# Kernel tuning notes

Hardware: AMD Instinct MI355X
Metric: run time of the kernel (lower is better)

## Reference

```python
import jax, jax.numpy as jnp
import numpy as np

H = 12          # num heads
D = 768         # embed dim
HD = D // H     # head dim
SCALE = HD ** -0.5
NEG = -(3.0 ** 39)  # matches torch's triu(1) * -3.0**39 mask value


def setup_inputs() -> dict:
    key = jax.random.key(0)
    ks = jax.random.split(key, 9)
    B, S = 4, 1024
    lim = 1.0 / np.sqrt(D)
    def lin(k):
        kw, kb = jax.random.split(k)
        W = jax.random.uniform(kw, (D, D), jnp.float32, -lim, lim)  # [out,in]
        b = jax.random.uniform(kb, (D,), jnp.float32, -lim, lim)
        return W, b
    Wq, bq = lin(ks[0]); Wk, bk = lin(ks[1]); Wv, bv = lin(ks[2]); Wo, bo = lin(ks[3])
    hidden_states = jax.random.normal(ks[4], (B, S, D), jnp.float32)
    return {"hidden_states": hidden_states,
            "Wq": Wq, "bq": bq, "Wk": Wk, "bk": bk,
            "Wv": Wv, "bv": bv, "Wo": Wo, "bo": bo}


def reference(hidden_states, Wq, bq, Wk, bk, Wv, bv, Wo, bo):
    B, S, _ = hidden_states.shape
    split = lambda x: x.reshape(B, S, H, HD).transpose(0, 2, 1, 3)  # [B,H,S,HD]
    q = split(hidden_states @ Wq.T + bq) * SCALE
    k = split(hidden_states @ Wk.T + bk)
    v = split(hidden_states @ Wv.T + bv)
    scores = jnp.einsum('bhqd,bhkd->bhqk', q, k)
    causal_mask = jnp.triu(jnp.full((S, S), NEG, hidden_states.dtype), k=1)
    scores = scores + causal_mask  # broadcast over [B,H]
    probs = jax.nn.softmax(scores, axis=-1)
    out = jnp.einsum('bhqk,bhkd->bhqd', probs, v)
    out = out.transpose(0, 2, 1, 3).reshape(B, S, H * HD)
    return out @ Wo.T + bo
```

## Files before the change

kernel.cpp:

```cpp
#include <hip/hip_runtime.h>

#define NH 12
#define DM 768
#define HD 64
#define BB 4
#define SS 1024
#define MTOT (BB*SS)
#define ATT_SCALE 0.125f
#define NEGMASK (-4.0525551530189755e18f)

typedef __attribute__((ext_vector_type(8))) short short8;
typedef __attribute__((ext_vector_type(4))) float floatx4;
typedef __attribute__((ext_vector_type(4))) unsigned short ushort4v;

__device__ __forceinline__ float bf2f(unsigned short u){
    union { unsigned int i; float f; } x; x.i = ((unsigned int)u) << 16; return x.f;
}
__device__ __forceinline__ unsigned short f2bf(float f){
    union { float f; unsigned int i; } x; x.f = f;
    unsigned int i = x.i;
    return (unsigned short)((i + 0x7FFFu + ((i >> 16) & 1u)) >> 16);
}

#define XQ4 (MTOT*DM/4)
#define WQ4 (DM*DM/4)

__global__ __launch_bounds__(256) void convert_bf16(
    const float* __restrict__ X,
    const float* __restrict__ Wq, const float* __restrict__ Wk,
    const float* __restrict__ Wv, const float* __restrict__ Wo,
    unsigned short* __restrict__ Xb,
    unsigned short* __restrict__ Wqb, unsigned short* __restrict__ Wkb,
    unsigned short* __restrict__ Wvb, unsigned short* __restrict__ Wob)
{
    const int idx = blockIdx.x * 256 + threadIdx.x;
    const float* s; unsigned short* d; int off;
    if (idx < XQ4) { s = X; d = Xb; off = idx; }
    else {
        const int r = idx - XQ4;
        const int wsel = r / WQ4;
        off = r - wsel * WQ4;
        s = (wsel==0)?Wq:(wsel==1)?Wk:(wsel==2)?Wv:Wo;
        d = (wsel==0)?Wqb:(wsel==1)?Wkb:(wsel==2)?Wvb:Wob;
    }
    const float4 v = ((const float4*)s)[off];
    ushort4v o;
    o[0] = f2bf(v.x); o[1] = f2bf(v.y); o[2] = f2bf(v.z); o[3] = f2bf(v.w);
    ((ushort4v*)d)[off] = o;
}

__global__ __launch_bounds__(256) void qkv_mfma(
    const unsigned short* __restrict__ Xb,
    const unsigned short* __restrict__ Wqb,
    const unsigned short* __restrict__ Wkb,
    const unsigned short* __restrict__ Wvb,
    const float* __restrict__ bq, const float* __restrict__ bk,
    const float* __restrict__ bv,
    unsigned short* __restrict__ qout,
    unsigned short* __restrict__ kout,
    unsigned short* __restrict__ vout)
{
    const int which = blockIdx.z;
    const int n0 = blockIdx.x * 64;
    const int m0 = blockIdx.y * 128;
    const unsigned short* W = (which==0) ? Wqb : (which==1) ? Wkb : Wvb;
    const float* bias = (which==0) ? bq : (which==1) ? bk : bv;
    const float scl = (which==0) ? ATT_SCALE : 1.0f;

    __shared__ unsigned short As[128*32];
    __shared__ unsigned short Bs[64*32];

    const int t = threadIdx.x;
    const int w = t >> 6, lane = t & 63;
    const int c = lane & 15, g = lane >> 4;
    const int wr = w >> 1, wc = w & 1;

    floatx4 acc[4][2] = {};

    const int srow = lane >> 2;
    const int ske  = (lane & 3) * 8;

    for (int k0 = 0; k0 < DM; k0 += 32) {
        __syncthreads();
        #pragma unroll
        for (int j = 0; j < 2; ++j) {
            const int row = w*32 + j*16 + srow;
            __builtin_amdgcn_global_load_lds(
                (const __attribute__((address_space(1))) unsigned int*)
                    (Xb + (size_t)(m0 + row) * DM + k0 + ske),
                (__attribute__((address_space(3))) unsigned int*)
                    (As + (w*32 + j*16) * 32),
                16, 0, 0);
        }
        {
            const int row = w*16 + srow;
            __builtin_amdgcn_global_load_lds(
                (const __attribute__((address_space(1))) unsigned int*)
                    (W + (size_t)(n0 + row) * DM + k0 + ske),
                (__attribute__((address_space(3))) unsigned int*)
                    (Bs + (w*16) * 32),
                16, 0, 0);
        }
        __syncthreads();

        short8 af[4], bfr[2];
        #pragma unroll
        for (int mi = 0; mi < 4; ++mi)
            af[mi] = *(const short8*)(As + (wr*64 + mi*16 + c)*32 + g*8);
        #pragma unroll
        for (int ni = 0; ni < 2; ++ni)
            bfr[ni] = *(const short8*)(Bs + (wc*32 + ni*16 + c)*32 + g*8);
        #pragma unroll
        for (int mi = 0; mi < 4; ++mi)
            #pragma unroll
            for (int ni = 0; ni < 2; ++ni)
                acc[mi][ni] = __builtin_amdgcn_mfma_f32_16x16x32_bf16(
                    af[mi], bfr[ni], acc[mi][ni], 0, 0, 0);
    }

    #pragma unroll
    for (int mi = 0; mi < 4; ++mi) {
        #pragma unroll
        for (int r = 0; r < 4; ++r) {
            const int m = m0 + wr*64 + mi*16 + g*4 + r;
            const int b = m >> 10, s = m & 1023;
            #pragma unroll
            for (int ni = 0; ni < 2; ++ni) {
                const int n = n0 + wc*32 + ni*16 + c;
                const int h = n >> 6, hd = n & 63;
                const float val = (acc[mi][ni][r] + bias[n]) * scl;
                if (which == 2)
                    vout[(((size_t)(b*NH + h))*HD + hd)*SS + s] = f2bf(val);
                else if (which == 1)
                    kout[(((size_t)(b*NH + h))*SS + s)*HD + hd] = f2bf(val);
                else
                    qout[(((size_t)(b*NH + h))*SS + s)*HD + hd] = f2bf(val);
            }
        }
    }
}

__global__ __launch_bounds__(64) void attn_mfma(
    const unsigned short* __restrict__ Q,
    const unsigned short* __restrict__ K,
    const unsigned short* __restrict__ VT,
    unsigned short* __restrict__ O)
{
    const int idx = blockIdx.x;
    const int bh  = idx % 48;
    const int z   = 63 - (idx / 48);
    const int q0  = z * 16;

    const unsigned short* Qp  = Q  + (size_t)bh * SS * HD;
    const unsigned short* Kp  = K  + (size_t)bh * SS * HD;
    const unsigned short* VTp = VT + (size_t)bh * HD * SS;

    __shared__ unsigned short Pl[16 * 72];

    const int lane = threadIdx.x;
    const int c    = lane & 15;
    const int g    = lane >> 4;

    short8 qf[2];
    #pragma unroll
    for (int st = 0; st < 2; ++st)
        qf[st] = *(const short8*)(Qp + (size_t)(q0 + c) * HD + g*8 + 32*st);

    floatx4 Oacc[4] = {};
    float m_r[4], l_r[4];
    #pragma unroll
    for (int r = 0; r < 4; ++r) { m_r[r] = -INFINITY; l_r[r] = 0.0f; }

    const int ntile = z/4 + 1;
    for (int kt = 0; kt < ntile; ++kt) {
        const int k0 = kt * 64;

        short8 kf[4][2], vf[2][4];
        #pragma unroll
        for (int nf = 0; nf < 4; ++nf)
            #pragma unroll
            for (int st = 0; st < 2; ++st)
                kf[nf][st] = *(const short8*)(Kp + (size_t)(k0 + nf*16 + c) * HD + g*8 + 32*st);
        #pragma unroll
        for (int st = 0; st < 2; ++st)
            #pragma unroll
            for (int nf = 0; nf < 4; ++nf)
                vf[st][nf] = *(const short8*)(VTp + (size_t)(nf*16 + c) * SS + k0 + g*8 + 32*st);

        floatx4 Sacc[4] = {};
        #pragma unroll
        for (int nf = 0; nf < 4; ++nf)
            #pragma unroll
            for (int st = 0; st < 2; ++st)
                Sacc[nf] = __builtin_amdgcn_mfma_f32_16x16x32_bf16(qf[st], kf[nf][st], Sacc[nf], 0, 0, 0);

        if (kt == ntile - 1) {
            #pragma unroll
            for (int nf = 0; nf < 4; ++nf) {
                const int col = k0 + nf*16 + c;
                #pragma unroll
                for (int r = 0; r < 4; ++r) {
                    const int row = q0 + g*4 + r;
                    if (col > row) Sacc[nf][r] += NEGMASK;
                }
            }
        }

        #pragma unroll
        for (int r = 0; r < 4; ++r) {
            float mx = fmaxf(fmaxf(Sacc[0][r], Sacc[1][r]),
                             fmaxf(Sacc[2][r], Sacc[3][r]));
            #pragma unroll
            for (int msk = 1; msk < 16; msk <<= 1)
                mx = fmaxf(mx, __shfl_xor(mx, msk, 64));
            const float mnew = fmaxf(m_r[r], mx);
            const float alpha = __expf(m_r[r] - mnew);
            float sum = 0.0f;
            #pragma unroll
            for (int nf = 0; nf < 4; ++nf) {
                const float p = __expf(Sacc[nf][r] - mnew);
                Sacc[nf][r] = p;
                sum += p;
            }
            #pragma unroll
            for (int msk = 1; msk < 16; msk <<= 1)
                sum += __shfl_xor(sum, msk, 64);
            l_r[r] = l_r[r] * alpha + sum;
            m_r[r] = mnew;
            #pragma unroll
            for (int nf = 0; nf < 4; ++nf) Oacc[nf][r] *= alpha;
        }

        #pragma unroll
        for (int r = 0; r < 4; ++r)
            #pragma unroll
            for (int nf = 0; nf < 4; ++nf)
                Pl[(g*4 + r) * 72 + nf*16 + c] = f2bf(Sacc[nf][r]);

        #pragma unroll
        for (int st = 0; st < 2; ++st) {
            const short8 pf = *(const short8*)(Pl + c * 72 + g*8 + 32*st);
            #pragma unroll
            for (int nf = 0; nf < 4; ++nf)
                Oacc[nf] = __builtin_amdgcn_mfma_f32_16x16x32_bf16(pf, vf[st][nf], Oacc[nf], 0, 0, 0);
        }
    }

    const int b = bh / NH, h = bh % NH;
    #pragma unroll
    for (int r = 0; r < 4; ++r) {
        const float inv = 1.0f / l_r[r];
        const int s = q0 + g*4 + r;
        #pragma unroll
        for (int nf = 0; nf < 4; ++nf)
            O[((size_t)(b*SS + s))*DM + h*HD + nf*16 + c] = f2bf(Oacc[nf][r] * inv);
    }
}

__global__ __launch_bounds__(256) void out_mfma(
    const unsigned short* __restrict__ A,
    const unsigned short* __restrict__ Wb,
    const float* __restrict__ bias,
    float* __restrict__ outf)
{
    const int n0 = blockIdx.x * 64;
    const int m0 = blockIdx.y * 128;

    __shared__ unsigned short As[128*32];
    __shared__ unsigned short Bs[64*32];

    const int t = threadIdx.x;
    const int w = t >> 6, lane = t & 63;
    const int c = lane & 15, g = lane >> 4;
    const int wr = w >> 1, wc = w & 1;

    floatx4 acc[4][2] = {};

    const int srow = lane >> 2;
    const int ske  = (lane & 3) * 8;

    for (int k0 = 0; k0 < DM; k0 += 32) {
        __syncthreads();
        #pragma unroll
        for (int j = 0; j < 2; ++j) {
            const int row = w*32 + j*16 + srow;
            __builtin_amdgcn_global_load_lds(
                (const __attribute__((address_space(1))) unsigned int*)
                    (A + (size_t)(m0 + row) * DM + k0 + ske),
                (__attribute__((address_space(3))) unsigned int*)
                    (As + (w*32 + j*16) * 32),
                16, 0, 0);
        }
        {
            const int row = w*16 + srow;
            __builtin_amdgcn_global_load_lds(
                (const __attribute__((address_space(1))) unsigned int*)
                    (Wb + (size_t)(n0 + row) * DM + k0 + ske),
                (__attribute__((address_space(3))) unsigned int*)
                    (Bs + (w*16) * 32),
                16, 0, 0);
        }
        __syncthreads();

        short8 af[4], bfr[2];
        #pragma unroll
        for (int mi = 0; mi < 4; ++mi)
            af[mi] = *(const short8*)(As + (wr*64 + mi*16 + c)*32 + g*8);
        #pragma unroll
        for (int ni = 0; ni < 2; ++ni)
            bfr[ni] = *(const short8*)(Bs + (wc*32 + ni*16 + c)*32 + g*8);
        #pragma unroll
        for (int mi = 0; mi < 4; ++mi)
            #pragma unroll
            for (int ni = 0; ni < 2; ++ni)
                acc[mi][ni] = __builtin_amdgcn_mfma_f32_16x16x32_bf16(
                    af[mi], bfr[ni], acc[mi][ni], 0, 0, 0);
    }

    #pragma unroll
    for (int mi = 0; mi < 4; ++mi) {
        #pragma unroll
        for (int r = 0; r < 4; ++r) {
            const int m = m0 + wr*64 + mi*16 + g*4 + r;
            #pragma unroll
            for (int ni = 0; ni < 2; ++ni) {
                const int n = n0 + wc*32 + ni*16 + c;
                outf[(size_t)m * DM + n] = acc[mi][ni][r] + bias[n];
            }
        }
    }
}

extern "C" void kernel_launch(void* const* d_in, const int* in_sizes, int n_in,
                              void* d_out, int out_size, void* d_ws, size_t ws_size,
                              hipStream_t stream) {
    const float* X  = (const float*)d_in[0];
    const float* Wq = (const float*)d_in[1];
    const float* bq = (const float*)d_in[2];
    const float* Wk = (const float*)d_in[3];
    const float* bk = (const float*)d_in[4];
    const float* Wv = (const float*)d_in[5];
    const float* bv = (const float*)d_in[6];
    const float* Wo = (const float*)d_in[7];
    const float* bo = (const float*)d_in[8];
    float* out = (float*)d_out;

    const size_t elems = (size_t)MTOT * DM;
    const size_t welems = (size_t)DM * DM;
    unsigned short* q    = (unsigned short*)d_ws;
    unsigned short* k    = q    + elems;
    unsigned short* vt   = k    + elems;
    unsigned short* attn = vt   + elems;
    unsigned short* xb   = attn + elems;
    unsigned short* wqb  = xb   + elems;
    unsigned short* wkb  = wqb  + welems;
    unsigned short* wvb  = wkb  + welems;
    unsigned short* wob  = wvb  + welems;

    convert_bf16<<<dim3((XQ4 + 4*WQ4) / 256), 256, 0, stream>>>(
        X, Wq, Wk, Wv, Wo, xb, wqb, wkb, wvb, wob);
    qkv_mfma<<<dim3(12, 32, 3), 256, 0, stream>>>(
        xb, wqb, wkb, wvb, bq, bk, bv, q, k, vt);
    attn_mfma<<<dim3(3072), 64, 0, stream>>>(q, k, vt, attn);
    out_mfma<<<dim3(12, 32), 256, 0, stream>>>(attn, wob, bo, out);
}
```

Measured before the change: 189.9 us.

## Double-buffer K/V fragments and transpose attention MFMA to column-per-lane softmax

The attention kernel now prefetches the next key/value tile into a second register buffer while the current tile is processed, overlapping global loads with MFMA and softmax work. The MFMA operands are swapped so each lane owns one query row. That turns the 16-lane shuffle reductions per row into two cross-group shuffles and lets the output be written as 4-element vector stores. The cost is higher register pressure from the doubled fragment buffers, which could reduce occupancy.

```diff
diff --git a/kernel.cpp b/kernel.cpp
--- a/kernel.cpp
+++ b/kernel.cpp
@@ -140,6 +140,86 @@
     }
 }
 
+__device__ __forceinline__ void attn_load_frags(
+    const unsigned short* __restrict__ Kp,
+    const unsigned short* __restrict__ VTp,
+    int k0, int c, int g, short8 (&kf)[4][2], short8 (&vf)[2][4])
+{
+    #pragma unroll
+    for (int nf = 0; nf < 4; ++nf)
+        #pragma unroll
+        for (int st = 0; st < 2; ++st) {
+            kf[nf][st] = *(const short8*)(Kp + (size_t)(k0 + nf*16 + c) * HD + g*8 + 32*st);
+            vf[st][nf] = *(const short8*)(VTp + (size_t)(nf*16 + c) * SS + k0 + g*8 + 32*st);
+        }
+}
+
+__device__ __forceinline__ void attn_process_tile(
+    const short8 (&kf)[4][2], const short8 (&vf)[2][4], const short8 (&qf)[2],
+    int k0, bool islast, int qg, int c, int g,
+    float& m_c, float& l_c, floatx4 (&Oacc)[4],
+    unsigned short* __restrict__ Pl)
+{
+    floatx4 S[4] = {};
+    #pragma unroll
+    for (int nf = 0; nf < 4; ++nf)
+        #pragma unroll
+        for (int st = 0; st < 2; ++st)
+            S[nf] = __builtin_amdgcn_mfma_f32_16x16x32_bf16(kf[nf][st], qf[st], S[nf], 0, 0, 0);
+
+    if (islast) {
+        #pragma unroll
+        for (int nf = 0; nf < 4; ++nf) {
+            #pragma unroll
+            for (int r = 0; r < 4; ++r) {
+                const int key = k0 + nf*16 + g*4 + r;
+                if (key > qg) S[nf][r] += NEGMASK;
+            }
+        }
+    }
+
+    float mx = -INFINITY;
+    #pragma unroll
+    for (int nf = 0; nf < 4; ++nf)
+        #pragma unroll
+        for (int r = 0; r < 4; ++r) mx = fmaxf(mx, S[nf][r]);
+    mx = fmaxf(mx, __shfl_xor(mx, 16, 64));
+    mx = fmaxf(mx, __shfl_xor(mx, 32, 64));
+    const float mnew = fmaxf(m_c, mx);
+    const float alpha = __expf(m_c - mnew);
+    float sum = 0.0f;
+    #pragma unroll
+    for (int nf = 0; nf < 4; ++nf)
+        #pragma unroll
+        for (int r = 0; r < 4; ++r) {
+            const float p = __expf(S[nf][r] - mnew);
+            S[nf][r] = p;
+            sum += p;
+        }
+    sum += __shfl_xor(sum, 16, 64);
+    sum += __shfl_xor(sum, 32, 64);
+    l_c = l_c * alpha + sum;
+    m_c = mnew;
+    #pragma unroll
+    for (int nf = 0; nf < 4; ++nf)
+        #pragma unroll
+        for (int r = 0; r < 4; ++r) Oacc[nf][r] *= alpha;
+
+    #pragma unroll
+    for (int nf = 0; nf < 4; ++nf)
+        #pragma unroll
+        for (int r = 0; r < 4; ++r)
+            Pl[c * 72 + nf*16 + g*4 + r] = f2bf(S[nf][r]);
+
+    #pragma unroll
+    for (int st = 0; st < 2; ++st) {
+        const short8 pf = *(const short8*)(Pl + c * 72 + g*8 + 32*st);
+        #pragma unroll
+        for (int nf = 0; nf < 4; ++nf)
+            Oacc[nf] = __builtin_amdgcn_mfma_f32_16x16x32_bf16(vf[st][nf], pf, Oacc[nf], 0, 0, 0);
+    }
+}
+
 __global__ __launch_bounds__(64) void attn_mfma(
     const unsigned short* __restrict__ Q,
     const unsigned short* __restrict__ K,
@@ -160,6 +240,7 @@
     const int lane = threadIdx.x;
     const int c    = lane & 15;
     const int g    = lane >> 4;
+    const int qg   = q0 + c;
 
     short8 qf[2];
     #pragma unroll
@@ -167,93 +248,32 @@
         qf[st] = *(const short8*)(Qp + (size_t)(q0 + c) * HD + g*8 + 32*st);
 
     floatx4 Oacc[4] = {};
-    float m_r[4], l_r[4];
-    #pragma unroll
-    for (int r = 0; r < 4; ++r) { m_r[r] = -INFINITY; l_r[r] = 0.0f; }
+    float m_c = -INFINITY, l_c = 0.0f;
 
     const int ntile = z/4 + 1;
-    for (int kt = 0; kt < ntile; ++kt) {
-        const int k0 = kt * 64;
-
-        short8 kf[4][2], vf[2][4];
-        #pragma unroll
-        for (int nf = 0; nf < 4; ++nf)
-            #pragma unroll
-            for (int st = 0; st < 2; ++st)
-                kf[nf][st] = *(const short8*)(Kp + (size_t)(k0 + nf*16 + c) * HD + g*8 + 32*st);
-        #pragma unroll
-        for (int st = 0; st < 2; ++st)
-            #pragma unroll
-            for (int nf = 0; nf < 4; ++nf)
-                vf[st][nf] = *(const short8*)(VTp + (size_t)(nf*16 + c) * SS + k0 + g*8 + 32*st);
-
-        floatx4 Sacc[4] = {};
-        #pragma unroll
-        for (int nf = 0; nf < 4; ++nf)
-            #pragma unroll
-            for (int st = 0; st < 2; ++st)
-                Sacc[nf] = __builtin_amdgcn_mfma_f32_16x16x32_bf16(qf[st], kf[nf][st], Sacc[nf], 0, 0, 0);
-
-        if (kt == ntile - 1) {
-            #pragma unroll
-            for (int nf = 0; nf < 4; ++nf) {
-                const int col = k0 + nf*16 + c;
-                #pragma unroll
-                for (int r = 0; r < 4; ++r) {
-                    const int row = q0 + g*4 + r;
-                    if (col > row) Sacc[nf][r] += NEGMASK;
-                }
-            }
-        }
-
-        #pragma unroll
-        for (int r = 0; r < 4; ++r) {
-            float mx = fmaxf(fmaxf(Sacc[0][r], Sacc[1][r]),
-                             fmaxf(Sacc[2][r], Sacc[3][r]));
-            #pragma unroll
-            for (int msk = 1; msk < 16; msk <<= 1)
-                mx = fmaxf(mx, __shfl_xor(mx, msk, 64));
-            const float mnew = fmaxf(m_r[r], mx);
-            const float alpha = __expf(m_r[r] - mnew);
-            float sum = 0.0f;
-            #pragma unroll
-            for (int nf = 0; nf < 4; ++nf) {
-                const float p = __expf(Sacc[nf][r] - mnew);
-                Sacc[nf][r] = p;
-                sum += p;
-            }
-            #pragma unroll
-            for (int msk = 1; msk < 16; msk <<= 1)
-                sum += __shfl_xor(sum, msk, 64);
-            l_r[r] = l_r[r] * alpha + sum;
-            m_r[r] = mnew;
-            #pragma unroll
-            for (int nf = 0; nf < 4; ++nf) Oacc[nf][r] *= alpha;
-        }
-
-        #pragma unroll
-        for (int r = 0; r < 4; ++r)
-            #pragma unroll
-            for (int nf = 0; nf < 4; ++nf)
-                Pl[(g*4 + r) * 72 + nf*16 + c] = f2bf(Sacc[nf][r]);
-
-        #pragma unroll
-        for (int st = 0; st < 2; ++st) {
-            const short8 pf = *(const short8*)(Pl + c * 72 + g*8 + 32*st);
-            #pragma unroll
-            for (int nf = 0; nf < 4; ++nf)
-                Oacc[nf] = __builtin_amdgcn_mfma_f32_16x16x32_bf16(pf, vf[st][nf], Oacc[nf], 0, 0, 0);
-        }
+
+    short8 ka[4][2], va[2][4], kb[4][2], vb[2][4];
+    attn_load_frags(Kp, VTp, 0, c, g, ka, va);
+
+    for (int kt = 0; kt < ntile; kt += 2) {
+        if (kt + 1 < ntile)
+            attn_load_frags(Kp, VTp, (kt+1)*64, c, g, kb, vb);
+        attn_process_tile(ka, va, qf, kt*64, kt == ntile-1, qg, c, g, m_c, l_c, Oacc, Pl);
+        if (kt + 1 >= ntile) break;
+        if (kt + 2 < ntile)
+            attn_load_frags(Kp, VTp, (kt+2)*64, c, g, ka, va);
+        attn_process_tile(kb, vb, qf, (kt+1)*64, kt+1 == ntile-1, qg, c, g, m_c, l_c, Oacc, Pl);
     }
 
     const int b = bh / NH, h = bh % NH;
-    #pragma unroll
-    for (int r = 0; r < 4; ++r) {
-        const float inv = 1.0f / l_r[r];
-        const int s = q0 + g*4 + r;
-        #pragma unroll
-        for (int nf = 0; nf < 4; ++nf)
-            O[((size_t)(b*SS + s))*DM + h*HD + nf*16 + c] = f2bf(Oacc[nf][r] * inv);
+    const float inv = 1.0f / l_c;
+    unsigned short* op = O + ((size_t)(b*SS + q0 + c))*DM + h*HD;
+    #pragma unroll
+    for (int nf = 0; nf < 4; ++nf) {
+        ushort4v o4;
+        #pragma unroll
+        for (int r = 0; r < 4; ++r) o4[r] = f2bf(Oacc[nf][r] * inv);
+        *(ushort4v*)(op + nf*16 + g*4) = o4;
     }
 }
 
```

New measurement: 187.3 us. About the same (-1.3%).
